# Kernel optimization log

Measured on AMD Instinct MI355X. Metric: run time of the kernel, lower is better.

The kernel has to match this reference:

```python
import jax, jax.numpy as jnp
import numpy as np

N, C_IN, D, K, C_OUT = 50000, 256, 25000, 16, 256


def setup_inputs() -> dict:
    key = jax.random.key(0)
    k1, k2, k3, k4 = jax.random.split(key, 4)
    x = jax.random.normal(k1, (N, C_IN), dtype=jnp.float32)
    symm_norm = jax.random.uniform(k2, (N,), dtype=jnp.float32)
    domains = jax.random.randint(k3, (D, K), 0, N, dtype=jnp.int64)
    # Linear params: in = 2*C_IN (order-1 transfer doubles channels), xavier-uniform
    fan_in, fan_out = 2 * C_IN, C_OUT
    limit = float(np.sqrt(6.0 / (fan_in + fan_out)))
    w = jax.random.uniform(k4, (2 * C_IN, C_OUT), dtype=jnp.float32,
                           minval=-limit, maxval=limit)
    b = jnp.zeros((C_OUT,), dtype=jnp.float32)
    return {"x": x, "symm_norm": symm_norm, "domains": domains, "w": w, "b": b}


def reference(x, symm_norm, domains, w, b):
    # symmetric normalization: outer(features, symm_norm) -> per-node scale
    xs = x * symm_norm[:, None]                      # [N, C]
    # transfer1 (ptensors1 over singleton domains -> ptensors1 over target domains):
    # gather node features into each target domain; the two order-1 linmaps
    # (identity, broadcast-of-sum over the singleton intersection) coincide.
    g = jnp.take(xs, domains, axis=0)                # [D, K, C]
    f = jnp.concatenate([g, g], axis=-1)             # [D, K, 2C]
    # linear projection
    y = jnp.einsum('dkc,co->dko', f, w) + b          # [D, K, C_OUT]
    return y
```

## Files before the change

### kernel.cpp

```cpp
#include <hip/hip_runtime.h>
#include <hip/hip_bf16.h>


#define GM 50000
#define GK 256
#define GN 256
#define BM 64
#define BN 64
#define BK 16

__global__ __launch_bounds__(256)
void gemm_z_kernel(const float* __restrict__ x,
                   const float* __restrict__ sn,
                   const float* __restrict__ w,
                   const float* __restrict__ b,
                   float* __restrict__ z) {
    __shared__ float As[BM][BK + 1];
    __shared__ float Bs[BK][BN];

    const int t  = threadIdx.x;
    const int tx = t & 15;
    const int ty = t >> 4;
    const int rowBase = blockIdx.x * BM;
    const int colBase = blockIdx.y * BN;

    float acc[4][4] = {};

    const int la_col = t & 15;
    const int la_row = t >> 4;
    const int lb_col = t & 63;
    const int lb_row = t >> 6;

    for (int k0 = 0; k0 < GK; k0 += BK) {
        #pragma unroll
        for (int i = 0; i < 4; ++i) {
            int r = la_row + i * 16;
            int m = rowBase + r;
            float v = 0.0f;
            if (m < GM) v = x[(size_t)m * GK + k0 + la_col] * sn[m];
            As[r][la_col] = v;
        }
        #pragma unroll
        for (int i = 0; i < 4; ++i) {
            int kk = lb_row + i * 4;
            int gk = k0 + kk;
            int gn = colBase + lb_col;
            Bs[kk][lb_col] = w[(size_t)gk * GN + gn] +
                             w[(size_t)(gk + 256) * GN + gn];
        }
        __syncthreads();

        #pragma unroll
        for (int kk = 0; kk < BK; ++kk) {
            float a[4], bb[4];
            #pragma unroll
            for (int i = 0; i < 4; ++i) a[i]  = As[ty * 4 + i][kk];
            #pragma unroll
            for (int j = 0; j < 4; ++j) bb[j] = Bs[kk][tx * 4 + j];
            #pragma unroll
            for (int i = 0; i < 4; ++i)
                #pragma unroll
                for (int j = 0; j < 4; ++j)
                    acc[i][j] += a[i] * bb[j];
        }
        __syncthreads();
    }

    const int gn0 = colBase + tx * 4;
    const float4 bias = *reinterpret_cast<const float4*>(&b[gn0]);
    #pragma unroll
    for (int i = 0; i < 4; ++i) {
        int m = rowBase + ty * 4 + i;
        if (m < GM) {
            float4 v;
            v.x = acc[i][0] + bias.x;
            v.y = acc[i][1] + bias.y;
            v.z = acc[i][2] + bias.z;
            v.w = acc[i][3] + bias.w;
            *reinterpret_cast<float4*>(&z[(size_t)m * GN + gn0]) = v;
        }
    }
}

__global__ __launch_bounds__(256)
void gather_kernel(const float* __restrict__ z,
                   const int* __restrict__ domains,
                   float* __restrict__ out,
                   int R) {
    const int r = blockIdx.x * 4 + (threadIdx.x >> 6);
    if (r >= R) return;
    const int c = (threadIdx.x & 63) * 4;
    const int n = domains[r];
    const float4 v = *reinterpret_cast<const float4*>(&z[(size_t)n * GN + c]);
    *reinterpret_cast<float4*>(&out[(size_t)r * GN + c]) = v;
}

extern "C" void kernel_launch(void* const* d_in, const int* in_sizes, int n_in,
                              void* d_out, int out_size, void* d_ws, size_t ws_size,
                              hipStream_t stream) {
    const float* x  = (const float*)d_in[0];
    const float* sn = (const float*)d_in[1];
    const int*   dm = (const int*)d_in[2];
    const float* w  = (const float*)d_in[3];
    const float* b  = (const float*)d_in[4];
    float* out = (float*)d_out;
    float* z   = (float*)d_ws;

    dim3 gemm_grid((GM + BM - 1) / BM, GN / BN);
    gemm_z_kernel<<<gemm_grid, 256, 0, stream>>>(x, sn, w, b, z);

    const int R = 25000 * 16;
    gather_kernel<<<(R + 3) / 4, 256, 0, stream>>>(z, dm, out, R);
}
```

Before: 600.5 us.

## Enlarge GEMM tiles to 128x128 with 8x8 register blocking and vectorized loads

Raises the GEMM block tile from 64x64 to 128x128, with each thread now accumulating an 8x8 sub-tile. Shared memory is transposed to a k-major A layout so fragments load as float4 from LDS, and global loads of x and w are vectorized to float4. The aim is more FMAs per shared-memory and global load, less redundant w traffic, and more arithmetic intensity in the FP32 GEMM. In exchange it uses more registers per thread and launches fewer blocks, and the A-tile transpose store may cause LDS bank conflicts.

Measured after the change: 586.7 us. -2.3%, faster.

```diff
diff --git a/kernel.cpp b/kernel.cpp
--- a/kernel.cpp
+++ b/kernel.cpp
@@ -1,22 +1,23 @@
 #include <hip/hip_runtime.h>
-#include <hip/hip_bf16.h>
 
 
 #define GM 50000
 #define GK 256
 #define GN 256
-#define BM 64
-#define BN 64
+#define BM 128
+#define BN 128
 #define BK 16
+#define LDA (BM + 4)
+#define LDB (BN + 4)
 
-__global__ __launch_bounds__(256)
+__global__ __launch_bounds__(256, 4)
 void gemm_z_kernel(const float* __restrict__ x,
                    const float* __restrict__ sn,
                    const float* __restrict__ w,
                    const float* __restrict__ b,
                    float* __restrict__ z) {
-    __shared__ float As[BM][BK + 1];
-    __shared__ float Bs[BK][BN];
+    __shared__ float As[BK][LDA];
+    __shared__ float Bs[BK][LDB];
 
     const int t  = threadIdx.x;
     const int tx = t & 15;
@@ -24,61 +25,76 @@
     const int rowBase = blockIdx.x * BM;
     const int colBase = blockIdx.y * BN;
 
-    float acc[4][4] = {};
+    const int a_m = t >> 2;
+    const int a_k = (t & 3) * 4;
+    const int b_k = t >> 5;
+    const int b_n = (t & 31) * 4;
 
-    const int la_col = t & 15;
-    const int la_row = t >> 4;
-    const int lb_col = t & 63;
-    const int lb_row = t >> 6;
+    float acc[8][8] = {};
 
     for (int k0 = 0; k0 < GK; k0 += BK) {
         #pragma unroll
-        for (int i = 0; i < 4; ++i) {
-            int r = la_row + i * 16;
-            int m = rowBase + r;
-            float v = 0.0f;
-            if (m < GM) v = x[(size_t)m * GK + k0 + la_col] * sn[m];
-            As[r][la_col] = v;
+        for (int h = 0; h < 2; ++h) {
+            const int mr = a_m + h * 64;
+            const int m  = rowBase + mr;
+            float4 v = make_float4(0.f, 0.f, 0.f, 0.f);
+            if (m < GM) {
+                v = *reinterpret_cast<const float4*>(&x[(size_t)m * GK + k0 + a_k]);
+                const float s = sn[m];
+                v.x *= s; v.y *= s; v.z *= s; v.w *= s;
+            }
+            As[a_k + 0][mr] = v.x;
+            As[a_k + 1][mr] = v.y;
+            As[a_k + 2][mr] = v.z;
+            As[a_k + 3][mr] = v.w;
         }
         #pragma unroll
-        for (int i = 0; i < 4; ++i) {
-            int kk = lb_row + i * 4;
-            int gk = k0 + kk;
-            int gn = colBase + lb_col;
-            Bs[kk][lb_col] = w[(size_t)gk * GN + gn] +
-                             w[(size_t)(gk + 256) * GN + gn];
+        for (int h = 0; h < 2; ++h) {
+            const int kk = b_k + h * 8;
+            const int gk = k0 + kk;
+            const int gn = colBase + b_n;
+            float4 v0 = *reinterpret_cast<const float4*>(&w[(size_t)gk * GN + gn]);
+            float4 v1 = *reinterpret_cast<const float4*>(&w[(size_t)(gk + 256) * GN + gn]);
+            v0.x += v1.x; v0.y += v1.y; v0.z += v1.z; v0.w += v1.w;
+            *reinterpret_cast<float4*>(&Bs[kk][b_n]) = v0;
         }
         __syncthreads();
 
         #pragma unroll
         for (int kk = 0; kk < BK; ++kk) {
-            float a[4], bb[4];
+            float a[8], bb[8];
+            *reinterpret_cast<float4*>(&a[0])  =
+                *reinterpret_cast<const float4*>(&As[kk][ty * 4]);
+            *reinterpret_cast<float4*>(&a[4])  =
+                *reinterpret_cast<const float4*>(&As[kk][64 + ty * 4]);
+            *reinterpret_cast<float4*>(&bb[0]) =
+                *reinterpret_cast<const float4*>(&Bs[kk][tx * 4]);
+            *reinterpret_cast<float4*>(&bb[4]) =
+                *reinterpret_cast<const float4*>(&Bs[kk][64 + tx * 4]);
             #pragma unroll
-            for (int i = 0; i < 4; ++i) a[i]  = As[ty * 4 + i][kk];
-            #pragma unroll
-            for (int j = 0; j < 4; ++j) bb[j] = Bs[kk][tx * 4 + j];
-            #pragma unroll
-            for (int i = 0; i < 4; ++i)
+            for (int i = 0; i < 8; ++i)
                 #pragma unroll
-                for (int j = 0; j < 4; ++j)
+                for (int j = 0; j < 8; ++j)
                     acc[i][j] += a[i] * bb[j];
         }
         __syncthreads();
     }
 
-    const int gn0 = colBase + tx * 4;
-    const float4 bias = *reinterpret_cast<const float4*>(&b[gn0]);
+    const int n0 = colBase + tx * 4;
+    const float4 bias0 = *reinterpret_cast<const float4*>(&b[n0]);
+    const float4 bias1 = *reinterpret_cast<const float4*>(&b[n0 + 64]);
     #pragma unroll
-    for (int i = 0; i < 4; ++i) {
-        int m = rowBase + ty * 4 + i;
-        if (m < GM) {
-            float4 v;
-            v.x = acc[i][0] + bias.x;
-            v.y = acc[i][1] + bias.y;
-            v.z = acc[i][2] + bias.z;
-            v.w = acc[i][3] + bias.w;
-            *reinterpret_cast<float4*>(&z[(size_t)m * GN + gn0]) = v;
-        }
+    for (int i = 0; i < 8; ++i) {
+        const int m = rowBase + (i >> 2) * 64 + ty * 4 + (i & 3);
+        if (m >= GM) continue;
+        float* zr = &z[(size_t)m * GN];
+        float4 v;
+        v.x = acc[i][0] + bias0.x; v.y = acc[i][1] + bias0.y;
+        v.z = acc[i][2] + bias0.z; v.w = acc[i][3] + bias0.w;
+        *reinterpret_cast<float4*>(&zr[n0]) = v;
+        v.x = acc[i][4] + bias1.x; v.y = acc[i][5] + bias1.y;
+        v.z = acc[i][6] + bias1.z; v.w = acc[i][7] + bias1.w;
+        *reinterpret_cast<float4*>(&zr[n0 + 64]) = v;
     }
 }
 
```
